# Kernel tuning notes

Hardware: AMD Instinct MI355X
Metric: run time of the kernel (lower is better)

Reference implementation:

```python
import jax, jax.numpy as jnp
import numpy as np

B, T, D, N, L = 8, 2048, 256, 64, 4
LN_EPS = 1e-5


def setup_inputs() -> dict:
    key = jax.random.key(0)
    ks = jax.random.split(key, 8)
    def rn(k, shape, scale=1.0):
        return jax.random.normal(k, shape, dtype=jnp.float32) * scale
    A_init = jnp.log(0.5 + jnp.arange(N, dtype=jnp.float32))  # (N,)
    inp = {
        "sequences": rn(ks[0], (B, T, D)),
        # per-layer stacked params (leading dim L)
        "Wi": rn(ks[1], (L, D, D), 1.0 / np.sqrt(D)),
        "bi": jnp.zeros((L, D), jnp.float32),
        "A_log": jnp.broadcast_to(A_init, (L, D, N)) + 0.0,
        "Cm": rn(ks[2], (L, D, N), 1.0 / np.sqrt(N)),
        "Dp": jnp.ones((L, D), jnp.float32),
        "log_dt": jax.random.uniform(ks[3], (L, D), jnp.float32) * (np.log(0.1) - np.log(0.001)) + np.log(0.001),
        "Wo": rn(ks[4], (L, D, D), 1.0 / np.sqrt(D)),
        "bo": jnp.zeros((L, D), jnp.float32),
        "ln1_g": jnp.ones((L, D), jnp.float32),
        "ln1_b": jnp.zeros((L, D), jnp.float32),
        "ln2_g": jnp.ones((L, D), jnp.float32),
        "ln2_b": jnp.zeros((L, D), jnp.float32),
        "W1": rn(ks[5], (L, D, 4 * D), 1.0 / np.sqrt(D)),
        "b1": jnp.zeros((L, 4 * D), jnp.float32),
        "W2": rn(ks[6], (L, 4 * D, D), 1.0 / np.sqrt(4 * D)),
        "b2": jnp.zeros((L, D), jnp.float32),
        "lnf_g": jnp.ones((D,), jnp.float32),
        "lnf_b": jnp.zeros((D,), jnp.float32),
    }
    return inp


def _ln(x, g, b):
    m = x.mean(-1, keepdims=True)
    v = x.var(-1, keepdims=True)
    return (x - m) / jnp.sqrt(v + LN_EPS) * g + b


def _s4_kernel(A_log_l, Cm_l, log_dt_l, Tlen):
    dt = jnp.exp(log_dt_l)                       # (D,)
    A = -jnp.exp(A_log_l)                        # (D,N)
    A_bar = jnp.exp(A * dt[:, None])             # (D,N)
    B_bar = (A_bar - 1.0) / (A * np.sqrt(N))     # (D,N)
    CB = Cm_l * B_bar                            # (D,N)
    logAb = jnp.log(jnp.clip(A_bar, 1e-10))
    powers = jnp.arange(Tlen, dtype=jnp.float32)
    # (D,N,T) power tensor contracted over N -> (D,T)
    return jnp.einsum('dn,dnt->dt', CB, jnp.exp(logAb[:, :, None] * powers))


def reference(sequences, Wi, bi, A_log, Cm, Dp, log_dt, Wo, bo,
              ln1_g, ln1_b, ln2_g, ln2_b, W1, b1, W2, b2, lnf_g, lnf_b):
    x = sequences  # dropout is identity in eval mode
    Tlen = x.shape[1]
    nfft = 2 * Tlen
    for l in range(L):
        # --- S4D sub-block (pre-norm) ---
        h = _ln(x, ln1_g[l], ln1_b[l])
        u = (h @ Wi[l] + bi[l]).transpose(0, 2, 1)   # (B,D,T)
        K = _s4_kernel(A_log[l], Cm[l], log_dt[l], Tlen)  # (D,T)
        u_f = jnp.fft.rfft(u, n=nfft, axis=-1)
        K_f = jnp.fft.rfft(K, n=nfft, axis=-1)
        y = jnp.fft.irfft(u_f * K_f[None], n=nfft, axis=-1)[..., :Tlen]
        y = y + Dp[l][None, :, None] * u
        y = y.transpose(0, 2, 1) @ Wo[l] + bo[l]
        x = x + y
        # --- MLP sub-block (pre-norm) ---
        h2 = _ln(x, ln2_g[l], ln2_b[l])
        x = x + (jax.nn.gelu(h2 @ W1[l] + b1[l], approximate=False) @ W2[l] + b2[l])
    return _ln(x, lnf_g, lnf_b)
```

## Files before the change

kernel.cpp:

```cpp
#include <hip/hip_runtime.h>
#include <hip/hip_bf16.h>

#define NB 8
#define TT 2048
#define DD 256
#define NN 64
#define LL 4
#define CC 32
#define GG 64
#define BT (NB*TT)

typedef __attribute__((ext_vector_type(8))) short short8;
typedef __attribute__((ext_vector_type(4))) short short4v;
typedef __attribute__((ext_vector_type(4))) float f32x4;

__device__ __forceinline__ float bf2f(__hip_bfloat16 v){ return __bfloat162float(v); }
__device__ __forceinline__ __hip_bfloat16 f2bf(float v){ return __float2bfloat16(v); }
__device__ __forceinline__ short f2bfbits(float v){
  __hip_bfloat16 h = __float2bfloat16(v);
  return __builtin_bit_cast(short, h);
}
__device__ __forceinline__ float bfbits2f(short s){
  __hip_bfloat16 h = __builtin_bit_cast(__hip_bfloat16, s);
  return __bfloat162float(h);
}

#define VMCNT(N) do{ asm volatile("s_waitcnt vmcnt(" #N ")" ::: "memory"); \
                     __builtin_amdgcn_sched_barrier(0); }while(0)
__device__ __forceinline__ void barrier_pre(){
  asm volatile("" ::: "memory");
  __builtin_amdgcn_s_barrier();
  asm volatile("" ::: "memory");
  __builtin_amdgcn_sched_barrier(0);
}
__device__ __forceinline__ void barrier_post(){
  asm volatile("s_waitcnt lgkmcnt(0)" ::: "memory");
  __builtin_amdgcn_sched_barrier(0);
  __builtin_amdgcn_s_barrier();
  asm volatile("" ::: "memory");
  __builtin_amdgcn_sched_barrier(0);
}

__device__ __forceinline__ int get_bf(const void* dtp){
  unsigned u = *(const unsigned*)dtp;
  return ((u >> 16) == (u & 0xFFFFu)) ? 1 : 0;
}

__device__ __forceinline__ float ldin(const void* p, size_t i, int bf){
  return bf ? __bfloat162float(((const __hip_bfloat16*)p)[i]) : ((const float*)p)[i];
}

__device__ __forceinline__ float gelu_f(float x){
  float y = 0.79788456f * fmaf(0.044715f, x*x*x, x);
  float e = __expf(-2.0f * fabsf(y));
  float t = (1.0f - e) / (1.0f + e);
  t = (y >= 0.0f) ? t : -t;
  return 0.5f * x * (1.0f + t);
}

__device__ __forceinline__ void async16(const void* g, void* l){
  __builtin_amdgcn_global_load_lds(
      (const __attribute__((address_space(1))) void*)(unsigned long long)g,
      (__attribute__((address_space(3))) void*)(unsigned long long)l,
      16, 0, 0);
}

__global__ __launch_bounds__(256) void cast_ln_kernel(const void* __restrict__ seq,
    __hip_bfloat16* __restrict__ x, __hip_bfloat16* __restrict__ hN,
    const void* __restrict__ g, const void* __restrict__ b,
    const void* __restrict__ dtp)
{
  int bf = get_bf(dtp);
  int lane = threadIdx.x & 63, w = threadIdx.x >> 6;
  int row = blockIdx.x * 4 + w;
  int c = lane * 4;
  size_t base = (size_t)row*DD + c;
  float v0 = ldin(seq, base+0, bf), v1 = ldin(seq, base+1, bf);
  float v2 = ldin(seq, base+2, bf), v3 = ldin(seq, base+3, bf);
  short4v xk; xk.x=f2bfbits(v0); xk.y=f2bfbits(v1); xk.z=f2bfbits(v2); xk.w=f2bfbits(v3);
  *(short4v*)(x + base) = xk;
  float s = v0+v1+v2+v3;
  #pragma unroll
  for (int o = 1; o < 64; o <<= 1) s += __shfl_xor(s, o);
  float mean = s * (1.0f/DD);
  float d0=v0-mean, d1=v1-mean, d2=v2-mean, d3=v3-mean;
  float sq = d0*d0+d1*d1+d2*d2+d3*d3;
  #pragma unroll
  for (int o = 1; o < 64; o <<= 1) sq += __shfl_xor(sq, o);
  float r = rsqrtf(sq * (1.0f/DD) + 1e-5f);
  short4v hk;
  hk.x = f2bfbits(d0*r*ldin(g,c+0,bf) + ldin(b,c+0,bf));
  hk.y = f2bfbits(d1*r*ldin(g,c+1,bf) + ldin(b,c+1,bf));
  hk.z = f2bfbits(d2*r*ldin(g,c+2,bf) + ldin(b,c+2,bf));
  hk.w = f2bfbits(d3*r*ldin(g,c+3,bf) + ldin(b,c+3,bf));
  *(short4v*)(hN + base) = hk;
}

__global__ __launch_bounds__(256) void transpose_all_kernel(
    const void* __restrict__ Wi, const void* __restrict__ Wo,
    const void* __restrict__ W1, const void* __restrict__ W2,
    __hip_bfloat16* __restrict__ WiT, __hip_bfloat16* __restrict__ WoT,
    __hip_bfloat16* __restrict__ W1T, __hip_bfloat16* __restrict__ W2T,
    const void* __restrict__ dtp)
{
  int bf = get_bf(dtp);
  __shared__ float tile[32][33];
  int id = blockIdx.x;
  const void* W; __hip_bfloat16* Wt; int K, N, l, n0, k0;
  if (id < 256){
    W=Wi; Wt=WiT; K=DD; N=DD;
    int t=id;       l=t>>6; int r=t&63;  n0=(r&7)*32;  k0=(r>>3)*32;
  } else if (id < 512){
    W=Wo; Wt=WoT; K=DD; N=DD;
    int t=id-256;   l=t>>6; int r=t&63;  n0=(r&7)*32;  k0=(r>>3)*32;
  } else if (id < 1536){
    W=W1; Wt=W1T; K=DD; N=4*DD;
    int t=id-512;   l=t>>8; int r=t&255; n0=(r&31)*32; k0=(r>>5)*32;
  } else {
    W=W2; Wt=W2T; K=4*DD; N=DD;
    int t=id-1536;  l=t>>8; int r=t&255; n0=(r&7)*32;  k0=(r>>3)*32;
  }
  size_t zoff = (size_t)l * K * N;
  int tx = threadIdx.x, ty = threadIdx.y;
  #pragma unroll
  for (int i = 0; i < 4; i++)
    tile[ty + i*8][tx] = ldin(W, zoff + (size_t)(k0 + ty + i*8)*N + n0 + tx, bf);
  __syncthreads();
  #pragma unroll
  for (int i = 0; i < 4; i++)
    Wt[zoff + (size_t)(n0 + ty + i*8)*K + k0 + tx] = f2bf(tile[tx][ty + i*8]);
}

__global__ __launch_bounds__(256) void gemm_w1_kernel(
    const __hip_bfloat16* __restrict__ A, const __hip_bfloat16* __restrict__ Wt,
    const void* __restrict__ bias, size_t boff,
    __hip_bfloat16* __restrict__ C, int N, int K, const void* __restrict__ dtp)
{
  int bf = get_bf(dtp);
  __shared__ __align__(16) char smem[49152];
  short (*Als)[2][128][32] = (short(*)[2][128][32])smem;
  short (*Bls)[2][64][32]  = (short(*)[2][64][32])(smem + 32768);
  short* Cls = (short*)smem;
  int tid = threadIdx.x;
  int lane = tid & 63, w = tid >> 6;
  int quad = lane >> 4, row16 = lane & 15;
  int wm = (w >> 1) * 64, wn = (w & 1) * 32;
  int bm = blockIdx.x * 128, bn = blockIdx.y * 64;
  const short* Ag = (const short*)A + (size_t)bm * K;
  const short* Bg = (const short*)Wt + (size_t)bn * K;
  int nt = K >> 6;
  {
    #pragma unroll
    for (int p = 0; p < 4; p++){
      int ch = p*256 + tid; int kc = ch>>9, r=(ch>>2)&127, c=(ch&3)*8;
      async16(Ag + (size_t)r*K + kc*32 + c, &Als[0][kc][r][c]);
    }
    #pragma unroll
    for (int p = 0; p < 2; p++){
      int c2 = p*256 + tid; int k2 = c2>>8, r2=(c2>>2)&63, cc=(c2&3)*8;
      async16(Bg + (size_t)r2*K + k2*32 + cc, &Bls[0][k2][r2][cc]);
    }
  }
  f32x4 acc[4][2] = {};
  for (int t = 0; t < nt; t++){
    int cur = t & 1;
    if (t + 1 < nt){
      int nb_ = cur ^ 1, k0 = (t+1) << 6;
      #pragma unroll
      for (int p = 0; p < 4; p++){
        int ch = p*256 + tid; int kc = ch>>9, r=(ch>>2)&127, c=(ch&3)*8;
        async16(Ag + (size_t)r*K + k0 + kc*32 + c, &Als[nb_][kc][r][c]);
      }
      #pragma unroll
      for (int p = 0; p < 2; p++){
        int c2 = p*256 + tid; int k2 = c2>>8, r2=(c2>>2)&63, cc=(c2&3)*8;
        async16(Bg + (size_t)r2*K + k0 + k2*32 + cc, &Bls[nb_][k2][r2][cc]);
      }
      VMCNT(6);
    } else {
      VMCNT(0);
    }
    barrier_pre();
    #pragma unroll
    for (int kc = 0; kc < 2; kc++){
      short8 af[4], bfr[2];
      #pragma unroll
      for (int i = 0; i < 4; i++)
        af[i] = *(const short8*)&Als[cur][kc][wm + i*16 + row16][quad*8];
      #pragma unroll
      for (int j = 0; j < 2; j++)
        bfr[j] = *(const short8*)&Bls[cur][kc][wn + j*16 + row16][quad*8];
      #pragma unroll
      for (int i = 0; i < 4; i++)
        #pragma unroll
        for (int j = 0; j < 2; j++)
          acc[i][j] = __builtin_amdgcn_mfma_f32_16x16x32_bf16(af[i], bfr[j], acc[i][j], 0, 0, 0);
    }
    barrier_post();
  }
  #pragma unroll
  for (int i = 0; i < 4; i++){
    #pragma unroll
    for (int j = 0; j < 2; j++){
      int col = wn + j*16 + row16;
      float bv = ldin(bias, boff + bn + col, bf);
      #pragma unroll
      for (int r = 0; r < 4; r++){
        int row = wm + i*16 + quad*4 + r;
        Cls[row*72 + col] = f2bfbits(gelu_f(acc[i][j][r] + bv));
      }
    }
  }
  __syncthreads();
  #pragma unroll
  for (int p = 0; p < 4; p++){
    int ch = p*256 + tid;
    int row = ch >> 3, c0 = (ch & 7) * 8;
    short8 v = *(const short8*)&Cls[row*72 + c0];
    *(short8*)&C[(size_t)(bm + row)*N + bn + c0] = v;
  }
}

__global__ __launch_bounds__(256) void gemm_wi_lf_kernel(
    const __hip_bfloat16* __restrict__ A, const __hip_bfloat16* __restrict__ Wt,
    const void* __restrict__ bias, size_t boff,
    __hip_bfloat16* __restrict__ uout, __hip_bfloat16* __restrict__ LFS,
    const float* __restrict__ abT, int K, const void* __restrict__ dtp)
{
  int bf = get_bf(dtp);
  __shared__ __align__(16) char smem[73728];
  short (*Als)[2][32][32]  = (short(*)[2][32][32])smem;
  short (*Bls)[2][256][32] = (short(*)[2][256][32])(smem + 8192);
  float* Cls = (float*)smem;
  int tid = threadIdx.x, lane = tid & 63, w = tid >> 6;
  int quad = lane >> 4, row16 = lane & 15;
  int wn = w * 64;
  int bm = blockIdx.x * 32;
  const short* Ag = (const short*)A + (size_t)bm * K;
  const short* Bg = (const short*)Wt;
  int nt = K >> 6;
  {
    int ch = tid; int kc = ch>>7, r=(ch>>2)&31, c=(ch&3)*8;
    async16(Ag + (size_t)r*K + kc*32 + c, &Als[0][kc][r][c]);
    #pragma unroll
    for (int p = 0; p < 8; p++){
      int c2 = p*256 + tid; int k2 = c2>>10, r2=(c2>>2)&255, cc=(c2&3)*8;
      async16(Bg + (size_t)r2*K + k2*32 + cc, &Bls[0][k2][r2][cc]);
    }
  }
  f32x4 acc[2][4] = {};
  for (int t = 0; t < nt; t++){
    int cur = t & 1;
    if (t + 1 < nt){
      int nb_ = cur ^ 1, k0 = (t+1) << 6;
      int ch = tid; int kc = ch>>7, r=(ch>>2)&31, c=(ch&3)*8;
      async16(Ag + (size_t)r*K + k0 + kc*32 + c, &Als[nb_][kc][r][c]);
      #pragma unroll
      for (int p = 0; p < 8; p++){
        int c2 = p*256 + tid; int k2 = c2>>10, r2=(c2>>2)&255, cc=(c2&3)*8;
        async16(Bg + (size_t)r2*K + k0 + k2*32 + cc, &Bls[nb_][k2][r2][cc]);
      }
      VMCNT(9);
    } else {
      VMCNT(0);
    }
    barrier_pre();
    #pragma unroll
    for (int kc = 0; kc < 2; kc++){
      short8 af[2], bfr[4];
      #pragma unroll
      for (int i = 0; i < 2; i++)
        af[i] = *(const short8*)&Als[cur][kc][i*16 + row16][quad*8];
      #pragma unroll
      for (int j = 0; j < 4; j++)
        bfr[j] = *(const short8*)&Bls[cur][kc][wn + j*16 + row16][quad*8];
      #pragma unroll
      for (int i = 0; i < 2; i++)
        #pragma unroll
        for (int j = 0; j < 4; j++)
          acc[i][j] = __builtin_amdgcn_mfma_f32_16x16x32_bf16(af[i], bfr[j], acc[i][j], 0, 0, 0);
    }
    barrier_post();
  }
  #pragma unroll
  for (int i = 0; i < 2; i++)
    #pragma unroll
    for (int j = 0; j < 4; j++){
      int col = wn + j*16 + row16;
      #pragma unroll
      for (int r = 0; r < 4; r++){
        int row = i*16 + quad*4 + r;
        Cls[row*260 + col] = acc[i][j][r];
      }
    }
  __syncthreads();
  {
    int row = tid >> 3, l7 = tid & 7;
    size_t rbase = (size_t)(bm + row)*DD;
    #pragma unroll
    for (int q = 0; q < 8; q++){
      int c0 = l7*4 + q*32;
      float4 t = *(const float4*)&Cls[row*260 + c0];
      float v0 = t.x + ldin(bias, boff+c0+0, bf);
      float v1 = t.y + ldin(bias, boff+c0+1, bf);
      float v2 = t.z + ldin(bias, boff+c0+2, bf);
      float v3 = t.w + ldin(bias, boff+c0+3, bf);
      float4 wbk; wbk.x=v0; wbk.y=v1; wbk.z=v2; wbk.w=v3;
      *(float4*)&Cls[row*260 + c0] = wbk;
      short4v pk; pk.x=f2bfbits(v0); pk.y=f2bfbits(v1); pk.z=f2bfbits(v2); pk.w=f2bfbits(v3);
      *(short4v*)&uout[rbase + c0] = pk;
    }
  }
  __syncthreads();
  {
    int d = tid;
    int cix = bm >> 5;
    float ab[NN], accn[NN];
    #pragma unroll
    for (int n = 0; n < NN; n++){ ab[n] = abT[n*DD + d]; accn[n] = 0.0f; }
    #pragma unroll 1
    for (int s = 0; s < CC; s++){
      float uv = Cls[s*260 + d];
      #pragma unroll
      for (int n = 0; n < NN; n++) accn[n] = fmaf(ab[n], accn[n], uv);
    }
    #pragma unroll
    for (int n = 0; n < NN; n++)
      LFS[((size_t)cix*NN + n)*DD + d] = f2bf(accn[n]);
  }
}

__global__ __launch_bounds__(256) void s4_scan_kernel(__hip_bfloat16* __restrict__ LFS,
    const float* __restrict__ AbarCT)
{
  int d = threadIdx.x;
  int n = blockIdx.x & (NN-1), b = blockIdx.x >> 6;
  float a = AbarCT[n*DD + d];
  size_t base = ((size_t)(b*GG)*NN + n)*DD + d;
  const size_t gs = (size_t)NN*DD;
  float s = 0.0f;
  #pragma unroll 1
  for (int g = 0; g < GG; g += 8){
    float lf[8];
    #pragma unroll
    for (int k = 0; k < 8; k++) lf[k] = bf2f(LFS[base + (size_t)(g+k)*gs]);
    #pragma unroll
    for (int k = 0; k < 8; k++){
      LFS[base + (size_t)(g+k)*gs] = f2bf(s);
      s = fmaf(a, s, lf[k]);
    }
  }
}

__global__ __launch_bounds__(512, 4) void gemm_wo_recur_kernel(
    const __hip_bfloat16* __restrict__ uB, const __hip_bfloat16* __restrict__ Sin,
    const float* __restrict__ abT, const float* __restrict__ cbT,
    const void* __restrict__ Dp, size_t dpoff,
    const __hip_bfloat16* __restrict__ Wt, const void* __restrict__ bias, size_t boff,
    const __hip_bfloat16* __restrict__ resx, __hip_bfloat16* __restrict__ xout,
    const void* __restrict__ g, size_t goff, const void* __restrict__ bb, size_t bboff,
    __hip_bfloat16* __restrict__ hout)
{
  int bf = get_bf(Dp);
  __shared__ __align__(16) char smem[50176];
  short* Uls   = (short*)smem;
  short* Afull = (short*)(smem + 16384);
  short* Bext  = (short*)(smem + 32768);
  float* Cls   = (float*)(smem + 16384);
  int tid = threadIdx.x, lane = tid & 63, w = tid >> 6;
  int quad = lane >> 4, row16 = lane & 15;
  int bm = blockIdx.x * CC;
  const short* Bg = (const short*)Wt;
  {
    const short* ug = (const short*)uB + (size_t)bm * DD;
    async16(ug + tid*8,        Uls + tid*8);
    async16(ug + 4096 + tid*8, Uls + 4096 + tid*8);
    #pragma unroll
    for (int p = 0; p < 2; p++){
      int ch = p*512 + tid; int r = ch >> 2, c = (ch & 3) * 8;
      async16(Bg + (size_t)r*DD + c, Bext + ch*8);
    }
  }
  int d = tid >> 1, ng = tid & 1, nb = ng * 32;
  float st[32], ab[32], cb[32];
  {
    const __hip_bfloat16* sbase = Sin + ((size_t)(bm >> 5) * NN + nb)*DD + d;
    const float* abase = abT + (size_t)nb*DD + d;
    const float* cbase = cbT + (size_t)nb*DD + d;
    #pragma unroll
    for (int i = 0; i < 32; i++){
      st[i] = bf2f(sbase[(size_t)i*DD]);
      ab[i] = abase[(size_t)i*DD];
      cb[i] = cbase[(size_t)i*DD];
    }
  }
  float dp = ldin(Dp, dpoff + d, bf);
  __syncthreads();
  {
    short* ya = Afull + (d >> 5)*1024 + (d & 31);
    float uv = bfbits2f(Uls[d]);
    #pragma unroll 1
    for (int tau = 0; tau < CC; tau++){
      float uvn = (tau < CC-1) ? bfbits2f(Uls[(tau+1)*DD + d]) : 0.0f;
      float a0 = 0.0f, a1 = 0.0f, a2 = 0.0f, a3 = 0.0f;
      #pragma unroll
      for (int i = 0; i < 32; i += 4){
        st[i+0] = fmaf(ab[i+0], st[i+0], uv); a0 = fmaf(cb[i+0], st[i+0], a0);
        st[i+1] = fmaf(ab[i+1], st[i+1], uv); a1 = fmaf(cb[i+1], st[i+1], a1);
        st[i+2] = fmaf(ab[i+2], st[i+2], uv); a2 = fmaf(cb[i+2], st[i+2], a2);
        st[i+3] = fmaf(ab[i+3], st[i+3], uv); a3 = fmaf(cb[i+3], st[i+3], a3);
      }
      float tot = (a0 + a1) + (a2 + a3);
      tot += __shfl_xor(tot, 1);
      if (ng == 0) ya[tau*32] = f2bfbits(fmaf(dp, uv, tot));
      uv = uvn;
    }
  }
  __syncthreads();
  int wn = w * 32;
  f32x4 acc[2][2] = {};
  #pragma unroll
  for (int t = 0; t < 8; t++){
    if (t < 7){
      short* nxt = ((t+1) & 1) ? Uls : Bext;
      #pragma unroll
      for (int p = 0; p < 2; p++){
        int ch = p*512 + tid; int r = ch >> 2, c = (ch & 3) * 8;
        async16(Bg + (size_t)r*DD + (t+1)*32 + c, nxt + ch*8);
      }
      VMCNT(2);
    } else {
      VMCNT(0);
    }
    barrier_pre();
    const short* cur = (t & 1) ? Uls : Bext;
    short8 af[2], bfr[2];
    #pragma unroll
    for (int i = 0; i < 2; i++)
      af[i] = *(const short8*)&Afull[t*1024 + (i*16 + row16)*32 + quad*8];
    #pragma unroll
    for (int j = 0; j < 2; j++)
      bfr[j] = *(const short8*)&cur[(wn + j*16 + row16)*32 + quad*8];
    #pragma unroll
    for (int i = 0; i < 2; i++)
      #pragma unroll
      for (int j = 0; j < 2; j++)
        acc[i][j] = __builtin_amdgcn_mfma_f32_16x16x32_bf16(af[i], bfr[j], acc[i][j], 0, 0, 0);
    barrier_post();
  }
  #pragma unroll
  for (int i = 0; i < 2; i++)
    #pragma unroll
    for (int j = 0; j < 2; j++){
      int col = wn + j*16 + row16;
      #pragma unroll
      for (int r = 0; r < 4; r++){
        int row = i*16 + quad*4 + r;
        Cls[row*260 + col] = acc[i][j][r];
      }
    }
  __syncthreads();
  int row = tid >> 4, l4 = tid & 15;
  size_t rbase = (size_t)(bm + row)*DD;
  float v[4][4];
  #pragma unroll
  for (int q = 0; q < 4; q++){
    int c0 = l4*4 + q*64;
    float4 t = *(const float4*)&Cls[row*260 + c0];
    short4v rx = *(const short4v*)&resx[rbase + c0];
    v[q][0] = t.x + ldin(bias, boff+c0+0, bf) + bfbits2f(rx.x);
    v[q][1] = t.y + ldin(bias, boff+c0+1, bf) + bfbits2f(rx.y);
    v[q][2] = t.z + ldin(bias, boff+c0+2, bf) + bfbits2f(rx.z);
    v[q][3] = t.w + ldin(bias, boff+c0+3, bf) + bfbits2f(rx.w);
    short4v pk; pk.x=f2bfbits(v[q][0]); pk.y=f2bfbits(v[q][1]);
    pk.z=f2bfbits(v[q][2]); pk.w=f2bfbits(v[q][3]);
    *(short4v*)&xout[rbase + c0] = pk;
  }
  float s = 0.0f, sq = 0.0f;
  #pragma unroll
  for (int q = 0; q < 4; q++)
    #pragma unroll
    for (int e = 0; e < 4; e++){ s += v[q][e]; sq += v[q][e]*v[q][e]; }
  #pragma unroll
  for (int o = 1; o < 16; o <<= 1){ s += __shfl_xor(s, o); sq += __shfl_xor(sq, o); }
  float mean = s * (1.0f/DD);
  float rstd = rsqrtf(sq * (1.0f/DD) - mean*mean + 1e-5f);
  #pragma unroll
  for (int q = 0; q < 4; q++){
    int c0 = l4*4 + q*64;
    short4v pk;
    pk.x = f2bfbits((v[q][0]-mean)*rstd*ldin(g,goff+c0+0,bf) + ldin(bb,bboff+c0+0,bf));
    pk.y = f2bfbits((v[q][1]-mean)*rstd*ldin(g,goff+c0+1,bf) + ldin(bb,bboff+c0+1,bf));
    pk.z = f2bfbits((v[q][2]-mean)*rstd*ldin(g,goff+c0+2,bf) + ldin(bb,bboff+c0+2,bf));
    pk.w = f2bfbits((v[q][3]-mean)*rstd*ldin(g,goff+c0+3,bf) + ldin(bb,bboff+c0+3,bf));
    *(short4v*)&hout[rbase + c0] = pk;
  }
}

template <int MODE>
__global__ __launch_bounds__(256) void gemm_row_kernel(
    const __hip_bfloat16* __restrict__ A, const __hip_bfloat16* __restrict__ Wt,
    const void* __restrict__ bias, size_t boff,
    const __hip_bfloat16* __restrict__ resx, __hip_bfloat16* __restrict__ xout,
    const void* __restrict__ g, size_t goff,
    const void* __restrict__ bb, size_t bboff,
    __hip_bfloat16* __restrict__ hout, void* __restrict__ vout,
    int K, const void* __restrict__ dtp)
{
  int bf = get_bf(dtp);
  __shared__ __align__(16) char smem[73728];
  short (*Als)[2][32][32]  = (short(*)[2][32][32])smem;
  short (*Bls)[2][256][32] = (short(*)[2][256][32])(smem + 8192);
  float* Cls = (float*)smem;
  int tid = threadIdx.x, lane = tid & 63, w = tid >> 6;
  int quad = lane >> 4, row16 = lane & 15;
  int wn = w * 64;
  int bm = blockIdx.x * 32;
  const short* Ag = (const short*)A + (size_t)bm * K;
  const short* Bg = (const short*)Wt;
  int nt = K >> 6;
  {
    int ch = tid; int kc = ch>>7, r=(ch>>2)&31, c=(ch&3)*8;
    async16(Ag + (size_t)r*K + kc*32 + c, &Als[0][kc][r][c]);
    #pragma unroll
    for (int p = 0; p < 8; p++){
      int c2 = p*256 + tid; int k2 = c2>>10, r2=(c2>>2)&255, cc=(c2&3)*8;
      async16(Bg + (size_t)r2*K + k2*32 + cc, &Bls[0][k2][r2][cc]);
    }
  }
  f32x4 acc[2][4] = {};
  for (int t = 0; t < nt; t++){
    int cur = t & 1;
    if (t + 1 < nt){
      int nb_ = cur ^ 1, k0 = (t+1) << 6;
      int ch = tid; int kc = ch>>7, r=(ch>>2)&31, c=(ch&3)*8;
      async16(Ag + (size_t)r*K + k0 + kc*32 + c, &Als[nb_][kc][r][c]);
      #pragma unroll
      for (int p = 0; p < 8; p++){
        int c2 = p*256 + tid; int k2 = c2>>10, r2=(c2>>2)&255, cc=(c2&3)*8;
        async16(Bg + (size_t)r2*K + k0 + k2*32 + cc, &Bls[nb_][k2][r2][cc]);
      }
      VMCNT(9);
    } else {
      VMCNT(0);
    }
    barrier_pre();
    #pragma unroll
    for (int kc = 0; kc < 2; kc++){
      short8 af[2], bfr[4];
      #pragma unroll
      for (int i = 0; i < 2; i++)
        af[i] = *(const short8*)&Als[cur][kc][i*16 + row16][quad*8];
      #pragma unroll
      for (int j = 0; j < 4; j++)
        bfr[j] = *(const short8*)&Bls[cur][kc][wn + j*16 + row16][quad*8];
      #pragma unroll
      for (int i = 0; i < 2; i++)
        #pragma unroll
        for (int j = 0; j < 4; j++)
          acc[i][j] = __builtin_amdgcn_mfma_f32_16x16x32_bf16(af[i], bfr[j], acc[i][j], 0, 0, 0);
    }
    barrier_post();
  }
  #pragma unroll
  for (int i = 0; i < 2; i++)
    #pragma unroll
    for (int j = 0; j < 4; j++){
      int col = wn + j*16 + row16;
      #pragma unroll
      for (int r = 0; r < 4; r++){
        int row = i*16 + quad*4 + r;
        Cls[row*260 + col] = acc[i][j][r];
      }
    }
  __syncthreads();
  int row = tid >> 3, l7 = tid & 7;
  size_t rbase = (size_t)(bm + row)*DD;
  float v[8][4];
  #pragma unroll
  for (int q = 0; q < 8; q++){
    int c0 = l7*4 + q*32;
    float4 t = *(const float4*)&Cls[row*260 + c0];
    short4v rx = *(const short4v*)&resx[rbase + c0];
    v[q][0] = t.x + ldin(bias, boff+c0+0, bf) + bfbits2f(rx.x);
    v[q][1] = t.y + ldin(bias, boff+c0+1, bf) + bfbits2f(rx.y);
    v[q][2] = t.z + ldin(bias, boff+c0+2, bf) + bfbits2f(rx.z);
    v[q][3] = t.w + ldin(bias, boff+c0+3, bf) + bfbits2f(rx.w);
    if (MODE == 1){
      short4v pk; pk.x=f2bfbits(v[q][0]); pk.y=f2bfbits(v[q][1]);
      pk.z=f2bfbits(v[q][2]); pk.w=f2bfbits(v[q][3]);
      *(short4v*)&xout[rbase + c0] = pk;
    }
  }
  float s = 0.0f, sq = 0.0f;
  #pragma unroll
  for (int q = 0; q < 8; q++)
    #pragma unroll
    for (int e = 0; e < 4; e++){ s += v[q][e]; sq += v[q][e]*v[q][e]; }
  #pragma unroll
  for (int o = 1; o < 8; o <<= 1){ s += __shfl_xor(s, o); sq += __shfl_xor(sq, o); }
  float mean = s * (1.0f/DD);
  float rstd = rsqrtf(sq * (1.0f/DD) - mean*mean + 1e-5f);
  #pragma unroll
  for (int q = 0; q < 8; q++){
    int c0 = l7*4 + q*32;
    float o0 = (v[q][0]-mean)*rstd*ldin(g,goff+c0+0,bf) + ldin(bb,bboff+c0+0,bf);
    float o1 = (v[q][1]-mean)*rstd*ldin(g,goff+c0+1,bf) + ldin(bb,bboff+c0+1,bf);
    float o2 = (v[q][2]-mean)*rstd*ldin(g,goff+c0+2,bf) + ldin(bb,bboff+c0+2,bf);
    float o3 = (v[q][3]-mean)*rstd*ldin(g,goff+c0+3,bf) + ldin(bb,bboff+c0+3,bf);
    if (MODE == 1){
      short4v pk; pk.x=f2bfbits(o0); pk.y=f2bfbits(o1); pk.z=f2bfbits(o2); pk.w=f2bfbits(o3);
      *(short4v*)&hout[rbase + c0] = pk;
    } else {
      if (bf){
        short4v pk; pk.x=f2bfbits(o0); pk.y=f2bfbits(o1); pk.z=f2bfbits(o2); pk.w=f2bfbits(o3);
        *(short4v*)&((__hip_bfloat16*)vout)[rbase + c0] = pk;
      } else {
        float4 pk; pk.x=o0; pk.y=o1; pk.z=o2; pk.w=o3;
        *(float4*)&((float*)vout)[rbase + c0] = pk;
      }
    }
  }
}

__global__ __launch_bounds__(256) void s4_setup_kernel(const void* __restrict__ A_log,
    const void* __restrict__ Cm, const void* __restrict__ log_dt,
    float* __restrict__ AbarT, float* __restrict__ AbarCT, float* __restrict__ cbT,
    const void* __restrict__ dtp)
{
  int bf = get_bf(dtp);
  int d = threadIdx.x, n = blockIdx.x, l = blockIdx.y;
  float dtv = expf(ldin(log_dt, (size_t)l*DD + d, bf));
  float A   = -expf(ldin(A_log, ((size_t)l*DD + d)*NN + n, bf));
  float ab  = expf(A * dtv);
  float bbv = (fabsf(A) > 1e-8f) ? (ab - 1.0f) / (A * 8.0f) : dtv * 0.125f;
  float cb  = ldin(Cm, ((size_t)l*DD + d)*NN + n, bf) * bbv;
  size_t o = ((size_t)l*NN + n)*DD + d;
  AbarT[o] = ab;
  cbT[o]   = cb;
  float p = ab;
  #pragma unroll
  for (int i = 0; i < 5; i++) p *= p;
  AbarCT[o] = p;
}

extern "C" void kernel_launch(void* const* d_in, const int* in_sizes, int n_in,
                              void* d_out, int out_size, void* d_ws, size_t ws_size,
                              hipStream_t stream) {
  const void* seq   = d_in[0];
  const void* Wi    = d_in[1];
  const void* bi    = d_in[2];
  const void* A_log = d_in[3];
  const void* Cm    = d_in[4];
  const void* Dp    = d_in[5];
  const void* logdt = d_in[6];
  const void* Wo    = d_in[7];
  const void* bo    = d_in[8];
  const void* ln1g  = d_in[9];
  const void* ln1b  = d_in[10];
  const void* ln2g  = d_in[11];
  const void* ln2b  = d_in[12];
  const void* W1    = d_in[13];
  const void* b1    = d_in[14];
  const void* W2    = d_in[15];
  const void* b2    = d_in[16];
  const void* lnfg  = d_in[17];
  const void* lnfb  = d_in[18];

  char* ws = (char*)d_ws;
  size_t off = 0;
  __hip_bfloat16* x   = (__hip_bfloat16*)(ws + off); off += (size_t)BT*DD*2;
  __hip_bfloat16* uB  = (__hip_bfloat16*)(ws + off); off += (size_t)BT*DD*2;
  __hip_bfloat16* hN  = (__hip_bfloat16*)(ws + off); off += (size_t)BT*DD*2;
  __hip_bfloat16* mid = (__hip_bfloat16*)(ws + off); off += (size_t)BT*4*DD*2;
  __hip_bfloat16* LFS = (__hip_bfloat16*)(ws + off); off += (size_t)NB*GG*NN*DD*2;
  __hip_bfloat16* WiT = (__hip_bfloat16*)(ws + off); off += (size_t)LL*DD*DD*2;
  __hip_bfloat16* WoT = (__hip_bfloat16*)(ws + off); off += (size_t)LL*DD*DD*2;
  __hip_bfloat16* W1T = (__hip_bfloat16*)(ws + off); off += (size_t)LL*DD*4*DD*2;
  __hip_bfloat16* W2T = (__hip_bfloat16*)(ws + off); off += (size_t)LL*4*DD*DD*2;
  float* AbarT  = (float*)(ws + off); off += (size_t)LL*NN*DD*4;
  float* AbarCT = (float*)(ws + off); off += (size_t)LL*NN*DD*4;
  float* cbT    = (float*)(ws + off); off += (size_t)LL*NN*DD*4;

  (void)in_sizes; (void)n_in; (void)out_size; (void)ws_size;

  cast_ln_kernel<<<BT/4, 256, 0, stream>>>(seq, x, hN, ln1g, ln1b, Dp);
  transpose_all_kernel<<<2560, dim3(32,8), 0, stream>>>(
      Wi, Wo, W1, W2, WiT, WoT, W1T, W2T, Dp);
  s4_setup_kernel<<<dim3(NN, LL), DD, 0, stream>>>(A_log, Cm, logdt, AbarT, AbarCT, cbT, Dp);

  for (int l = 0; l < LL; l++){
    const size_t oD  = (size_t)l*DD;
    const size_t o4D = (size_t)l*4*DD;
    const float* abT  = AbarT  + (size_t)l*NN*DD;
    const float* abCT = AbarCT + (size_t)l*NN*DD;
    const float* cbTl = cbT    + (size_t)l*NN*DD;

    gemm_wi_lf_kernel<<<BT/32, 256, 0, stream>>>(
        hN, WiT + (size_t)l*DD*DD, bi, oD, uB, LFS, abT, DD, Dp);
    s4_scan_kernel<<<NB*NN, 256, 0, stream>>>(LFS, abCT);
    gemm_wo_recur_kernel<<<BT/32, 512, 0, stream>>>(
        uB, LFS, abT, cbTl, Dp, oD,
        WoT + (size_t)l*DD*DD, bo, oD, x, x,
        ln2g, oD, ln2b, oD, hN);

    gemm_w1_kernel<<<dim3(BT/128, 4*DD/64), 256, 0, stream>>>(
        hN, W1T + (size_t)l*DD*4*DD, b1, o4D, mid, 4*DD, DD, Dp);
    if (l < LL-1){
      gemm_row_kernel<1><<<BT/32, 256, 0, stream>>>(
          mid, W2T + (size_t)l*4*DD*DD, b2, oD, x, x,
          ln1g, (size_t)(l+1)*DD, ln1b, (size_t)(l+1)*DD, hN, nullptr, 4*DD, Dp);
    } else {
      gemm_row_kernel<2><<<BT/32, 256, 0, stream>>>(
          mid, W2T + (size_t)l*4*DD*DD, b2, oD, x, nullptr,
          lnfg, 0, lnfb, 0, nullptr, d_out, 4*DD, Dp);
    }
  }
}
```

Baseline: 587.0 us.

## Retile W2 row GEMM to 64-row blocks with 512 threads and K=32 stages

The W2 GEMM with fused residual and LayerNorm now has each block compute 64 rows using 8 waves in a 2x4 layout, instead of 32 rows with 4 waves. The K step per stage drops from 64 to 32, which shrinks shared memory from 72KB to 40KB. Each loaded W2 tile is now reused across twice as many rows, halving the weight traffic per row. The grid is halved, there are twice as many pipeline iterations with barriers, and the epilogue handles its two 32-row halves one after the other with extra syncs.

```diff
diff --git a/kernel.cpp b/kernel.cpp
--- a/kernel.cpp
+++ b/kernel.cpp
@@ -498,7 +498,7 @@
 }
 
 template <int MODE>
-__global__ __launch_bounds__(256) void gemm_row_kernel(
+__global__ __launch_bounds__(512) void gemm_row_kernel(
     const __hip_bfloat16* __restrict__ A, const __hip_bfloat16* __restrict__ Wt,
     const void* __restrict__ bias, size_t boff,
     const __hip_bfloat16* __restrict__ resx, __hip_bfloat16* __restrict__ xout,
@@ -508,118 +508,122 @@
     int K, const void* __restrict__ dtp)
 {
   int bf = get_bf(dtp);
-  __shared__ __align__(16) char smem[73728];
-  short (*Als)[2][32][32]  = (short(*)[2][32][32])smem;
-  short (*Bls)[2][256][32] = (short(*)[2][256][32])(smem + 8192);
+  __shared__ __align__(16) char smem[40960];
+  short (*Als)[64][32]  = (short(*)[64][32])smem;
+  short (*Bls)[256][32] = (short(*)[256][32])(smem + 8192);
   float* Cls = (float*)smem;
   int tid = threadIdx.x, lane = tid & 63, w = tid >> 6;
   int quad = lane >> 4, row16 = lane & 15;
-  int wn = w * 64;
-  int bm = blockIdx.x * 32;
+  int wm = (w >> 2) * 32, wn = (w & 3) * 64;
+  int bm = blockIdx.x * 64;
   const short* Ag = (const short*)A + (size_t)bm * K;
   const short* Bg = (const short*)Wt;
-  int nt = K >> 6;
+  int nt = K >> 5;
+  int rA = (tid & 255) >> 2, cA = (tid & 3) * 8;
   {
-    int ch = tid; int kc = ch>>7, r=(ch>>2)&31, c=(ch&3)*8;
-    async16(Ag + (size_t)r*K + kc*32 + c, &Als[0][kc][r][c]);
-    #pragma unroll
-    for (int p = 0; p < 8; p++){
-      int c2 = p*256 + tid; int k2 = c2>>10, r2=(c2>>2)&255, cc=(c2&3)*8;
-      async16(Bg + (size_t)r2*K + k2*32 + cc, &Bls[0][k2][r2][cc]);
+    async16(Ag + (size_t)rA*K + cA, &Als[0][rA][cA]);
+    #pragma unroll
+    for (int p = 0; p < 2; p++){
+      int ch = p*512 + tid; int r2 = ch >> 2, c2 = (ch & 3) * 8;
+      async16(Bg + (size_t)r2*K + c2, &Bls[0][r2][c2]);
     }
   }
   f32x4 acc[2][4] = {};
   for (int t = 0; t < nt; t++){
     int cur = t & 1;
     if (t + 1 < nt){
-      int nb_ = cur ^ 1, k0 = (t+1) << 6;
-      int ch = tid; int kc = ch>>7, r=(ch>>2)&31, c=(ch&3)*8;
-      async16(Ag + (size_t)r*K + k0 + kc*32 + c, &Als[nb_][kc][r][c]);
-      #pragma unroll
-      for (int p = 0; p < 8; p++){
-        int c2 = p*256 + tid; int k2 = c2>>10, r2=(c2>>2)&255, cc=(c2&3)*8;
-        async16(Bg + (size_t)r2*K + k0 + k2*32 + cc, &Bls[nb_][k2][r2][cc]);
-      }
-      VMCNT(9);
+      int nb_ = cur ^ 1, k0 = (t+1) << 5;
+      async16(Ag + (size_t)rA*K + k0 + cA, &Als[nb_][rA][cA]);
+      #pragma unroll
+      for (int p = 0; p < 2; p++){
+        int ch = p*512 + tid; int r2 = ch >> 2, c2 = (ch & 3) * 8;
+        async16(Bg + (size_t)r2*K + k0 + c2, &Bls[nb_][r2][c2]);
+      }
+      VMCNT(3);
     } else {
       VMCNT(0);
     }
     barrier_pre();
-    #pragma unroll
-    for (int kc = 0; kc < 2; kc++){
-      short8 af[2], bfr[4];
-      #pragma unroll
-      for (int i = 0; i < 2; i++)
-        af[i] = *(const short8*)&Als[cur][kc][i*16 + row16][quad*8];
+    short8 af[2], bfr[4];
+    #pragma unroll
+    for (int i = 0; i < 2; i++)
+      af[i] = *(const short8*)&Als[cur][wm + i*16 + row16][quad*8];
+    #pragma unroll
+    for (int j = 0; j < 4; j++)
+      bfr[j] = *(const short8*)&Bls[cur][wn + j*16 + row16][quad*8];
+    #pragma unroll
+    for (int i = 0; i < 2; i++)
       #pragma unroll
       for (int j = 0; j < 4; j++)
-        bfr[j] = *(const short8*)&Bls[cur][kc][wn + j*16 + row16][quad*8];
+        acc[i][j] = __builtin_amdgcn_mfma_f32_16x16x32_bf16(af[i], bfr[j], acc[i][j], 0, 0, 0);
+    barrier_post();
+  }
+  #pragma unroll 1
+  for (int h = 0; h < 2; h++){
+    if ((w >> 2) == h){
       #pragma unroll
       for (int i = 0; i < 2; i++)
         #pragma unroll
-        for (int j = 0; j < 4; j++)
-          acc[i][j] = __builtin_amdgcn_mfma_f32_16x16x32_bf16(af[i], bfr[j], acc[i][j], 0, 0, 0);
-    }
-    barrier_post();
-  }
-  #pragma unroll
-  for (int i = 0; i < 2; i++)
-    #pragma unroll
-    for (int j = 0; j < 4; j++){
-      int col = wn + j*16 + row16;
-      #pragma unroll
-      for (int r = 0; r < 4; r++){
-        int row = i*16 + quad*4 + r;
-        Cls[row*260 + col] = acc[i][j][r];
-      }
-    }
-  __syncthreads();
-  int row = tid >> 3, l7 = tid & 7;
-  size_t rbase = (size_t)(bm + row)*DD;
-  float v[8][4];
-  #pragma unroll
-  for (int q = 0; q < 8; q++){
-    int c0 = l7*4 + q*32;
-    float4 t = *(const float4*)&Cls[row*260 + c0];
-    short4v rx = *(const short4v*)&resx[rbase + c0];
-    v[q][0] = t.x + ldin(bias, boff+c0+0, bf) + bfbits2f(rx.x);
-    v[q][1] = t.y + ldin(bias, boff+c0+1, bf) + bfbits2f(rx.y);
-    v[q][2] = t.z + ldin(bias, boff+c0+2, bf) + bfbits2f(rx.z);
-    v[q][3] = t.w + ldin(bias, boff+c0+3, bf) + bfbits2f(rx.w);
-    if (MODE == 1){
-      short4v pk; pk.x=f2bfbits(v[q][0]); pk.y=f2bfbits(v[q][1]);
-      pk.z=f2bfbits(v[q][2]); pk.w=f2bfbits(v[q][3]);
-      *(short4v*)&xout[rbase + c0] = pk;
-    }
-  }
-  float s = 0.0f, sq = 0.0f;
-  #pragma unroll
-  for (int q = 0; q < 8; q++)
-    #pragma unroll
-    for (int e = 0; e < 4; e++){ s += v[q][e]; sq += v[q][e]*v[q][e]; }
-  #pragma unroll
-  for (int o = 1; o < 8; o <<= 1){ s += __shfl_xor(s, o); sq += __shfl_xor(sq, o); }
-  float mean = s * (1.0f/DD);
-  float rstd = rsqrtf(sq * (1.0f/DD) - mean*mean + 1e-5f);
-  #pragma unroll
-  for (int q = 0; q < 8; q++){
-    int c0 = l7*4 + q*32;
-    float o0 = (v[q][0]-mean)*rstd*ldin(g,goff+c0+0,bf) + ldin(bb,bboff+c0+0,bf);
-    float o1 = (v[q][1]-mean)*rstd*ldin(g,goff+c0+1,bf) + ldin(bb,bboff+c0+1,bf);
-    float o2 = (v[q][2]-mean)*rstd*ldin(g,goff+c0+2,bf) + ldin(bb,bboff+c0+2,bf);
-    float o3 = (v[q][3]-mean)*rstd*ldin(g,goff+c0+3,bf) + ldin(bb,bboff+c0+3,bf);
-    if (MODE == 1){
-      short4v pk; pk.x=f2bfbits(o0); pk.y=f2bfbits(o1); pk.z=f2bfbits(o2); pk.w=f2bfbits(o3);
-      *(short4v*)&hout[rbase + c0] = pk;
-    } else {
-      if (bf){
-        short4v pk; pk.x=f2bfbits(o0); pk.y=f2bfbits(o1); pk.z=f2bfbits(o2); pk.w=f2bfbits(o3);
-        *(short4v*)&((__hip_bfloat16*)vout)[rbase + c0] = pk;
-      } else {
-        float4 pk; pk.x=o0; pk.y=o1; pk.z=o2; pk.w=o3;
-        *(float4*)&((float*)vout)[rbase + c0] = pk;
-      }
-    }
+        for (int j = 0; j < 4; j++){
+          int col = wn + j*16 + row16;
+          #pragma unroll
+          for (int r = 0; r < 4; r++){
+            int rl = i*16 + quad*4 + r;
+            Cls[rl*260 + col] = acc[i][j][r];
+          }
+        }
+    }
+    __syncthreads();
+    {
+      int row = tid >> 4, l4 = tid & 15;
+      size_t rbase = (size_t)(bm + h*32 + row)*DD;
+      float v[4][4];
+      #pragma unroll
+      for (int q = 0; q < 4; q++){
+        int c0 = l4*4 + q*64;
+        float4 t = *(const float4*)&Cls[row*260 + c0];
+        short4v rx = *(const short4v*)&resx[rbase + c0];
+        v[q][0] = t.x + ldin(bias, boff+c0+0, bf) + bfbits2f(rx.x);
+        v[q][1] = t.y + ldin(bias, boff+c0+1, bf) + bfbits2f(rx.y);
+        v[q][2] = t.z + ldin(bias, boff+c0+2, bf) + bfbits2f(rx.z);
+        v[q][3] = t.w + ldin(bias, boff+c0+3, bf) + bfbits2f(rx.w);
+        if (MODE == 1){
+          short4v pk; pk.x=f2bfbits(v[q][0]); pk.y=f2bfbits(v[q][1]);
+          pk.z=f2bfbits(v[q][2]); pk.w=f2bfbits(v[q][3]);
+          *(short4v*)&xout[rbase + c0] = pk;
+        }
+      }
+      float s = 0.0f, sq = 0.0f;
+      #pragma unroll
+      for (int q = 0; q < 4; q++)
+        #pragma unroll
+        for (int e = 0; e < 4; e++){ s += v[q][e]; sq += v[q][e]*v[q][e]; }
+      #pragma unroll
+      for (int o = 1; o < 16; o <<= 1){ s += __shfl_xor(s, o); sq += __shfl_xor(sq, o); }
+      float mean = s * (1.0f/DD);
+      float rstd = rsqrtf(sq * (1.0f/DD) - mean*mean + 1e-5f);
+      #pragma unroll
+      for (int q = 0; q < 4; q++){
+        int c0 = l4*4 + q*64;
+        float o0 = (v[q][0]-mean)*rstd*ldin(g,goff+c0+0,bf) + ldin(bb,bboff+c0+0,bf);
+        float o1 = (v[q][1]-mean)*rstd*ldin(g,goff+c0+1,bf) + ldin(bb,bboff+c0+1,bf);
+        float o2 = (v[q][2]-mean)*rstd*ldin(g,goff+c0+2,bf) + ldin(bb,bboff+c0+2,bf);
+        float o3 = (v[q][3]-mean)*rstd*ldin(g,goff+c0+3,bf) + ldin(bb,bboff+c0+3,bf);
+        if (MODE == 1){
+          short4v pk; pk.x=f2bfbits(o0); pk.y=f2bfbits(o1); pk.z=f2bfbits(o2); pk.w=f2bfbits(o3);
+          *(short4v*)&hout[rbase + c0] = pk;
+        } else {
+          if (bf){
+            short4v pk; pk.x=f2bfbits(o0); pk.y=f2bfbits(o1); pk.z=f2bfbits(o2); pk.w=f2bfbits(o3);
+            *(short4v*)&((__hip_bfloat16*)vout)[rbase + c0] = pk;
+          } else {
+            float4 pk; pk.x=o0; pk.y=o1; pk.z=o2; pk.w=o3;
+            *(float4*)&((float*)vout)[rbase + c0] = pk;
+          }
+        }
+      }
+    }
+    __syncthreads();
   }
 }
 
@@ -707,11 +711,11 @@
     gemm_w1_kernel<<<dim3(BT/128, 4*DD/64), 256, 0, stream>>>(
         hN, W1T + (size_t)l*DD*4*DD, b1, o4D, mid, 4*DD, DD, Dp);
     if (l < LL-1){
-      gemm_row_kernel<1><<<BT/32, 256, 0, stream>>>(
+      gemm_row_kernel<1><<<BT/64, 512, 0, stream>>>(
           mid, W2T + (size_t)l*4*DD*DD, b2, oD, x, x,
           ln1g, (size_t)(l+1)*DD, ln1b, (size_t)(l+1)*DD, hN, nullptr, 4*DD, Dp);
     } else {
-      gemm_row_kernel<2><<<BT/32, 256, 0, stream>>>(
+      gemm_row_kernel<2><<<BT/64, 512, 0, stream>>>(
           mid, W2T + (size_t)l*4*DD*DD, b2, oD, x, nullptr,
           lnfg, 0, lnfb, 0, nullptr, d_out, 4*DD, Dp);
     }
```

Measured after the change: 595.1 us. Within noise of the previous version (+1.4%).
